# Optimization experiments

Measured on AMD Instinct MI355X. Metric: run time of the kernel, lower is better.

## Reference

```python
import jax, jax.numpy as jnp
import numpy as np

D_MODEL = 1024
NUM_HEADS = 16
D_K = D_MODEL // NUM_HEADS
SCALE = float(np.sqrt(D_K))


def setup_inputs() -> dict:
    key = jax.random.key(0)
    ks = jax.random.split(key, 12)
    B, S = 4, 2048
    s = 1.0 / np.sqrt(D_MODEL)
    inp = {
        'query': jax.random.normal(ks[0], (B, S, D_MODEL), jnp.float32),
        'key':   jax.random.normal(ks[1], (B, S, D_MODEL), jnp.float32),
        'value': jax.random.normal(ks[2], (B, S, D_MODEL), jnp.float32),
        'Wq': jax.random.normal(ks[3], (D_MODEL, D_MODEL), jnp.float32) * s,
        'bq': jax.random.normal(ks[4], (D_MODEL,), jnp.float32) * s,
        'Wk': jax.random.normal(ks[5], (D_MODEL, D_MODEL), jnp.float32) * s,
        'bk': jax.random.normal(ks[6], (D_MODEL,), jnp.float32) * s,
        'Wv': jax.random.normal(ks[7], (D_MODEL, D_MODEL), jnp.float32) * s,
        'bv': jax.random.normal(ks[8], (D_MODEL,), jnp.float32) * s,
        'Wo': jax.random.normal(ks[9], (D_MODEL, D_MODEL), jnp.float32) * s,
        'bo': jax.random.normal(ks[10], (D_MODEL,), jnp.float32) * s,
    }
    return inp


def reference(query, key, value, Wq, bq, Wk, bk, Wv, bv, Wo, bo):
    B, Sq, _ = query.shape
    Skv = key.shape[1]
    # torch Linear: x @ W.T + b
    def proj(x, W, b, S):
        y = jnp.einsum('bsd,ed->bse', x, W) + b
        return y.reshape(B, S, NUM_HEADS, D_K).transpose(0, 2, 1, 3)  # [B,H,S,dk]
    Q = proj(query, Wq, bq, Sq)
    K = proj(key, Wk, bk, Skv)
    V = proj(value, Wv, bv, Skv)
    scores = jnp.einsum('bhqd,bhkd->bhqk', Q, K) / SCALE  # [B,H,Sq,Skv]
    attn = jax.nn.softmax(scores, axis=-1)  # dropout=0 -> identity
    out = jnp.einsum('bhqk,bhkd->bhqd', attn, V)
    out = out.transpose(0, 2, 1, 3).reshape(B, Sq, D_MODEL)
    out = jnp.einsum('bsd,ed->bse', out, Wo) + bo
    return out
```

## Files before the change

kernel.cpp:

```cpp
#include <hip/hip_runtime.h>


typedef __attribute__((ext_vector_type(8))) __bf16 bf16x8;
typedef __attribute__((ext_vector_type(4))) __bf16 bf16x4;
typedef __attribute__((ext_vector_type(4))) float f32x4;

#define SCALE_FOLD 0.18033688011112043f

__device__ __forceinline__ void async_copy16(const void* g, void* lds) {
  __builtin_amdgcn_global_load_lds(
      (const __attribute__((address_space(1))) void*)g,
      (__attribute__((address_space(3))) void*)lds, 16, 0, 0);
}

template <int ROWS, int WIDTH>
__device__ __forceinline__ void stage_tile(const __bf16* __restrict__ g, int ld,
                                           __bf16* lds, int tid) {
  constexpr int CH = WIDTH / 8;
  const int wave_base = tid & ~63;
#pragma unroll
  for (int r = 0; r < ROWS * CH / 256; ++r) {
    int slot = r * 256 + tid;
    int row = slot / CH;
    int c = slot % CH;
    int gc = c ^ (row & (CH - 1));
    async_copy16(g + row * ld + gc * 8, lds + (r * 256 + wave_base) * 8);
  }
}

template <int WIDTH>
__device__ __forceinline__ bf16x8 frag_ld(const __bf16* lds, int row, int chunk) {
  return *(const bf16x8*)(lds + row * WIDTH +
                          ((chunk ^ (row & (WIDTH / 8 - 1))) << 3));
}

__global__ void cvt_all(const float* __restrict__ s0, const float* __restrict__ s1,
                        const float* __restrict__ s2, const float* __restrict__ s3,
                        const float* __restrict__ s4, const float* __restrict__ s5,
                        const float* __restrict__ s6, __bf16* d0, __bf16* d1,
                        __bf16* d2, __bf16* d3, __bf16* d4, __bf16* d5,
                        __bf16* d6, int n4_big, int n4_small) {
  const int z = blockIdx.y;
  const float* src;
  __bf16* dst;
  int n4;
  switch (z) {
    case 0: src = s0; dst = d0; n4 = n4_big; break;
    case 1: src = s1; dst = d1; n4 = n4_big; break;
    case 2: src = s2; dst = d2; n4 = n4_big; break;
    case 3: src = s3; dst = d3; n4 = n4_small; break;
    case 4: src = s4; dst = d4; n4 = n4_small; break;
    case 5: src = s5; dst = d5; n4 = n4_small; break;
    default: src = s6; dst = d6; n4 = n4_small; break;
  }
  int i = blockIdx.x * blockDim.x + threadIdx.x;
  if (i < n4) {
    float4 v = ((const float4*)src)[i];
    bf16x4 o = {(__bf16)v.x, (__bf16)v.y, (__bf16)v.z, (__bf16)v.w};
    ((bf16x4*)dst)[i] = o;
  }
}

__device__ __forceinline__ void gemm_body(const __bf16* __restrict__ A,
                                          const __bf16* __restrict__ B,
                                          const float* __restrict__ bias,
                                          void* __restrict__ out, int K,
                                          int mode, int m0, int n0,
                                          __bf16* Alds, __bf16* Blds) {
  const int tid = threadIdx.x;
  const int lane = tid & 63;
  const int w = tid >> 6;
  const int wm = w >> 1, wn = w & 1;
  const int l15 = lane & 15, quad = lane >> 4;

  f32x4 acc[4][4] = {};

  for (int k0 = 0; k0 < K; k0 += 64) {
    stage_tile<128, 64>(A + m0 * K + k0, K, Alds, tid);
    stage_tile<128, 64>(B + n0 * K + k0, K, Blds, tid);
    __syncthreads();
#pragma unroll
    for (int kc = 0; kc < 2; ++kc) {
      bf16x8 af[4], bfr[4];
#pragma unroll
      for (int mi = 0; mi < 4; ++mi)
        af[mi] = frag_ld<64>(Alds, wm * 64 + mi * 16 + l15, kc * 4 + quad);
#pragma unroll
      for (int ni = 0; ni < 4; ++ni)
        bfr[ni] = frag_ld<64>(Blds, wn * 64 + ni * 16 + l15, kc * 4 + quad);
#pragma unroll
      for (int mi = 0; mi < 4; ++mi)
#pragma unroll
        for (int ni = 0; ni < 4; ++ni)
          acc[mi][ni] = __builtin_amdgcn_mfma_f32_16x16x32_bf16(
              af[mi], bfr[ni], acc[mi][ni], 0, 0, 0);
    }
    __syncthreads();
  }

#pragma unroll
  for (int mi = 0; mi < 4; ++mi) {
#pragma unroll
    for (int i = 0; i < 4; ++i) {
      int grow = m0 + wm * 64 + mi * 16 + quad * 4 + i;
#pragma unroll
      for (int ni = 0; ni < 4; ++ni) {
        int gcol = n0 + wn * 64 + ni * 16 + l15;
        float v = acc[mi][ni][i];
        if (mode == 3) {
          v += bias[gcol];
          ((float*)out)[grow * 1024 + gcol] = v;
        } else if (mode == 2) {
          v += bias[grow];
          int h = grow >> 6, dd = grow & 63;
          int b = gcol >> 11, s = gcol & 2047;
          ((__bf16*)out)[(((b * 16 + h) * 64 + dd) * 2048) + s] = (__bf16)v;
        } else {
          v += bias[gcol];
          if (mode == 0) v *= SCALE_FOLD;
          int h = gcol >> 6, dd = gcol & 63;
          int b = grow >> 11, s = grow & 2047;
          ((__bf16*)out)[(((b * 16 + h) * 2048 + s) * 64) + dd] = (__bf16)v;
        }
      }
    }
  }
}

__global__ __launch_bounds__(256) void gemm_qkv(
    const __bf16* __restrict__ xq, const __bf16* __restrict__ xk,
    const __bf16* __restrict__ xv, const __bf16* __restrict__ wq,
    const __bf16* __restrict__ wk, const __bf16* __restrict__ wv,
    const float* __restrict__ bq, const float* __restrict__ bk,
    const float* __restrict__ bv, __bf16* Qb, __bf16* Kb, __bf16* Vtb) {
  __shared__ alignas(16) __bf16 Alds[128 * 64];
  __shared__ alignas(16) __bf16 Blds[128 * 64];
  const int z = blockIdx.z;
  if (z == 0) {
    gemm_body(xq, wq, bq, Qb, 1024, 0, blockIdx.y * 128, blockIdx.x * 128,
              Alds, Blds);
  } else if (z == 1) {
    gemm_body(xk, wk, bk, Kb, 1024, 1, blockIdx.y * 128, blockIdx.x * 128,
              Alds, Blds);
  } else {
    gemm_body(wv, xv, bv, Vtb, 1024, 2, blockIdx.x * 128, blockIdx.y * 128,
              Alds, Blds);
  }
}

__global__ __launch_bounds__(256) void gemm_out(const __bf16* __restrict__ A,
                                                const __bf16* __restrict__ B,
                                                const float* __restrict__ bias,
                                                float* __restrict__ out) {
  __shared__ alignas(16) __bf16 Alds[128 * 64];
  __shared__ alignas(16) __bf16 Blds[128 * 64];
  gemm_body(A, B, bias, out, 1024, 3, blockIdx.y * 128, blockIdx.x * 128, Alds,
            Blds);
}

__global__ __launch_bounds__(256) void attn_kernel(
    const __bf16* __restrict__ Qg, const __bf16* __restrict__ Kg,
    const __bf16* __restrict__ Vt, __bf16* __restrict__ AO) {
  __shared__ alignas(16) __bf16 Klds[2][64 * 64];
  __shared__ alignas(16) __bf16 Vlds[2][64 * 64];
  __shared__ alignas(16) __bf16 Plds[4][32 * 32];

  const int tid = threadIdx.x;
  const int lane = tid & 63;
  const int w = tid >> 6;
  const int l15 = lane & 15, quad = lane >> 4;
  const int bh = blockIdx.y;
  const int q0 = blockIdx.x * 128;
  const int S = 2048;

  const __bf16* Qbase = Qg + (size_t)bh * S * 64;
  const __bf16* Kbase = Kg + (size_t)bh * S * 64;
  const __bf16* Vbase = Vt + (size_t)bh * 64 * S;

  stage_tile<128, 64>(Qbase + q0 * 64, 64, (__bf16*)Klds, tid);
  __syncthreads();
  bf16x8 qf[2][2];
#pragma unroll
  for (int qi = 0; qi < 2; ++qi)
#pragma unroll
    for (int kc = 0; kc < 2; ++kc)
      qf[qi][kc] =
          frag_ld<64>((__bf16*)Klds, w * 32 + qi * 16 + l15, kc * 4 + quad);
  __syncthreads();

  stage_tile<64, 64>(Kbase, 64, Klds[0], tid);
  stage_tile<64, 64>(Vbase, S, Vlds[0], tid);
  __syncthreads();

  const bf16x8 ones = {__bf16(1.f), __bf16(1.f), __bf16(1.f), __bf16(1.f),
                       __bf16(1.f), __bf16(1.f), __bf16(1.f), __bf16(1.f)};

  f32x4 oacc[2][4] = {};
  f32x4 lacc[2] = {};
  __bf16* Pw = Plds[w];

  for (int mt = 0; mt < 32; ++mt) {
    const int cur = mt & 1;
    if (mt + 1 < 32) {
      stage_tile<64, 64>(Kbase + (mt + 1) * 64 * 64, 64, Klds[cur ^ 1], tid);
      stage_tile<64, 64>(Vbase + (mt + 1) * 64, S, Vlds[cur ^ 1], tid);
    }

#pragma unroll
    for (int sub = 0; sub < 2; ++sub) {
      f32x4 sacc[2][2] = {};
#pragma unroll
      for (int kc = 0; kc < 2; ++kc) {
        bf16x8 kf[2];
#pragma unroll
        for (int ci = 0; ci < 2; ++ci)
          kf[ci] =
              frag_ld<64>(Klds[cur], sub * 32 + ci * 16 + l15, kc * 4 + quad);
#pragma unroll
        for (int ci = 0; ci < 2; ++ci)
#pragma unroll
          for (int qi = 0; qi < 2; ++qi)
            sacc[ci][qi] = __builtin_amdgcn_mfma_f32_16x16x32_bf16(
                kf[ci], qf[qi][kc], sacc[ci][qi], 0, 0, 0);
      }

#pragma unroll
      for (int ci = 0; ci < 2; ++ci) {
#pragma unroll
        for (int qi = 0; qi < 2; ++qi) {
          bf16x4 pk;
#pragma unroll
          for (int i = 0; i < 4; ++i)
            pk[i] = (__bf16)__builtin_amdgcn_exp2f(sacc[ci][qi][i]);
          int qrow = qi * 16 + l15;
          int addr = qrow * 32 +
                     ((((ci << 1) + (quad >> 1)) ^ (qrow & 3)) << 3) +
                     ((quad & 1) << 2);
          *(bf16x4*)(Pw + addr) = pk;
        }
      }

      bf16x8 pf[2], vf[4];
#pragma unroll
      for (int mi = 0; mi < 2; ++mi)
        pf[mi] = frag_ld<32>(Pw, mi * 16 + l15, quad);
#pragma unroll
      for (int ni = 0; ni < 4; ++ni)
        vf[ni] = frag_ld<64>(Vlds[cur], ni * 16 + l15, sub * 4 + quad);
#pragma unroll
      for (int mi = 0; mi < 2; ++mi)
        lacc[mi] = __builtin_amdgcn_mfma_f32_16x16x32_bf16(pf[mi], ones,
                                                           lacc[mi], 0, 0, 0);
#pragma unroll
      for (int mi = 0; mi < 2; ++mi)
#pragma unroll
        for (int ni = 0; ni < 4; ++ni)
          oacc[mi][ni] = __builtin_amdgcn_mfma_f32_16x16x32_bf16(
              pf[mi], vf[ni], oacc[mi][ni], 0, 0, 0);
    }
    __syncthreads();
  }

  const int b = bh >> 4;
  const int hh = bh & 15;
#pragma unroll
  for (int mi = 0; mi < 2; ++mi) {
#pragma unroll
    for (int i = 0; i < 4; ++i) {
      int s = q0 + w * 32 + mi * 16 + quad * 4 + i;
      float inv_l = 1.f / lacc[mi][i];
#pragma unroll
      for (int ni = 0; ni < 4; ++ni) {
        int d = ni * 16 + l15;
        AO[((size_t)(b * 2048 + s)) * 1024 + hh * 64 + d] =
            (__bf16)(oacc[mi][ni][i] * inv_l);
      }
    }
  }
}

extern "C" void kernel_launch(void* const* d_in, const int* in_sizes, int n_in,
                              void* d_out, int out_size, void* d_ws,
                              size_t ws_size, hipStream_t stream) {
  const float* q_in = (const float*)d_in[0];
  const float* k_in = (const float*)d_in[1];
  const float* v_in = (const float*)d_in[2];
  const float* Wq = (const float*)d_in[3];
  const float* bq = (const float*)d_in[4];
  const float* Wk = (const float*)d_in[5];
  const float* bk = (const float*)d_in[6];
  const float* Wv = (const float*)d_in[7];
  const float* bv = (const float*)d_in[8];
  const float* Wo = (const float*)d_in[9];
  const float* bo = (const float*)d_in[10];

  const size_t SZ_X = (size_t)8192 * 1024 * 2;
  const size_t SZ_W = (size_t)1024 * 1024 * 2;
  char* p = (char*)d_ws;
  __bf16* xq = (__bf16*)p; p += SZ_X;
  __bf16* xk = (__bf16*)p; p += SZ_X;
  __bf16* xv = (__bf16*)p; p += SZ_X;
  __bf16* wqb = (__bf16*)p; p += SZ_W;
  __bf16* wkb = (__bf16*)p; p += SZ_W;
  __bf16* wvb = (__bf16*)p; p += SZ_W;
  __bf16* wob = (__bf16*)p; p += SZ_W;
  __bf16* Qb = (__bf16*)p; p += SZ_X;
  __bf16* Kb = (__bf16*)p; p += SZ_X;
  __bf16* Vtb = (__bf16*)p; p += SZ_X;
  __bf16* AOb = (__bf16*)p; p += SZ_X;

  const int nx4 = 8192 * 1024 / 4, nw4 = 1024 * 1024 / 4;
  cvt_all<<<dim3(nx4 / 256, 7), 256, 0, stream>>>(
      q_in, k_in, v_in, Wq, Wk, Wv, Wo, xq, xk, xv, wqb, wkb, wvb, wob, nx4,
      nw4);

  gemm_qkv<<<dim3(8, 64, 3), 256, 0, stream>>>(xq, xk, xv, wqb, wkb, wvb, bq,
                                               bk, bv, Qb, Kb, Vtb);

  attn_kernel<<<dim3(16, 64), 256, 0, stream>>>(Qb, Kb, Vtb, AOb);

  gemm_out<<<dim3(8, 64), 256, 0, stream>>>(AOb, wob, bo, (float*)d_out);
}
```

Baseline: 360.7 us.

## Rewrite attention as single-wave blocks with register-prefetched K/V

The attention kernel moves from 256-thread blocks that stage K/V tiles through LDS with block barriers to 64-thread single-wave blocks. Each wave handles 64 query rows, loads K and V fragments directly from global memory into registers, and double-buffers them one 32-key step ahead. The block index is remapped so that consecutive blocks hit different batch-head pairs. This removes LDS staging and __syncthreads, but the four waves that shared a K/V tile now each read it from global separately, relying on cache, and register pressure goes up.

Result: slower. 381.9 us (+5.9%).

```diff
diff --git a/kernel.cpp b/kernel.cpp
--- a/kernel.cpp
+++ b/kernel.cpp
@@ -158,116 +158,115 @@
             Blds);
 }
 
-__global__ __launch_bounds__(256) void attn_kernel(
+__global__ __launch_bounds__(64, 2) void attn_kernel(
     const __bf16* __restrict__ Qg, const __bf16* __restrict__ Kg,
     const __bf16* __restrict__ Vt, __bf16* __restrict__ AO) {
-  __shared__ alignas(16) __bf16 Klds[2][64 * 64];
-  __shared__ alignas(16) __bf16 Vlds[2][64 * 64];
-  __shared__ alignas(16) __bf16 Plds[4][32 * 32];
-
-  const int tid = threadIdx.x;
-  const int lane = tid & 63;
-  const int w = tid >> 6;
+  __shared__ alignas(16) __bf16 P[64 * 64];
+
+  const int lane = threadIdx.x;
   const int l15 = lane & 15, quad = lane >> 4;
-  const int bh = blockIdx.y;
-  const int q0 = blockIdx.x * 128;
   const int S = 2048;
 
-  const __bf16* Qbase = Qg + (size_t)bh * S * 64;
-  const __bf16* Kbase = Kg + (size_t)bh * S * 64;
-  const __bf16* Vbase = Vt + (size_t)bh * 64 * S;
-
-  stage_tile<128, 64>(Qbase + q0 * 64, 64, (__bf16*)Klds, tid);
-  __syncthreads();
-  bf16x8 qf[2][2];
-#pragma unroll
-  for (int qi = 0; qi < 2; ++qi)
+  const int bid = blockIdx.x;
+  const int bh = (bid & 7) * 8 + ((bid >> 3) & 7);
+  const int q0 = (bid >> 6) * 64;
+
+  const __bf16* Qb = Qg + (size_t)bh * S * 64 + q0 * 64;
+  const __bf16* Kb = Kg + (size_t)bh * S * 64;
+  const __bf16* Vb = Vt + (size_t)bh * 64 * S;
+
+  bf16x8 qf[4][2];
+#pragma unroll
+  for (int qi = 0; qi < 4; ++qi)
 #pragma unroll
     for (int kc = 0; kc < 2; ++kc)
       qf[qi][kc] =
-          frag_ld<64>((__bf16*)Klds, w * 32 + qi * 16 + l15, kc * 4 + quad);
-  __syncthreads();
-
-  stage_tile<64, 64>(Kbase, 64, Klds[0], tid);
-  stage_tile<64, 64>(Vbase, S, Vlds[0], tid);
-  __syncthreads();
+          *(const bf16x8*)(Qb + (qi * 16 + l15) * 64 + kc * 32 + quad * 8);
 
   const bf16x8 ones = {__bf16(1.f), __bf16(1.f), __bf16(1.f), __bf16(1.f),
                        __bf16(1.f), __bf16(1.f), __bf16(1.f), __bf16(1.f)};
 
-  f32x4 oacc[2][4] = {};
-  f32x4 lacc[2] = {};
-  __bf16* Pw = Plds[w];
-
-  for (int mt = 0; mt < 32; ++mt) {
-    const int cur = mt & 1;
-    if (mt + 1 < 32) {
-      stage_tile<64, 64>(Kbase + (mt + 1) * 64 * 64, 64, Klds[cur ^ 1], tid);
-      stage_tile<64, 64>(Vbase + (mt + 1) * 64, S, Vlds[cur ^ 1], tid);
-    }
-
-#pragma unroll
-    for (int sub = 0; sub < 2; ++sub) {
-      f32x4 sacc[2][2] = {};
-#pragma unroll
-      for (int kc = 0; kc < 2; ++kc) {
-        bf16x8 kf[2];
+  f32x4 oacc[4][4] = {};
+  f32x4 lacc[4] = {};
+
+  bf16x8 kf[2][2][2];
+  bf16x8 vf[2][4];
+
+#pragma unroll
+  for (int kc = 0; kc < 2; ++kc)
+#pragma unroll
+    for (int ci = 0; ci < 2; ++ci)
+      kf[0][kc][ci] =
+          *(const bf16x8*)(Kb + (ci * 16 + l15) * 64 + kc * 32 + quad * 8);
+#pragma unroll
+  for (int ni = 0; ni < 4; ++ni)
+    vf[0][ni] = *(const bf16x8*)(Vb + (ni * 16 + l15) * S + quad * 8);
+
+#pragma unroll 2
+  for (int t = 0; t < 64; ++t) {
+    const int cur = t & 1;
+    if (t + 1 < 64) {
+      const int kv1 = (t + 1) * 32;
+#pragma unroll
+      for (int kc = 0; kc < 2; ++kc)
 #pragma unroll
         for (int ci = 0; ci < 2; ++ci)
-          kf[ci] =
-              frag_ld<64>(Klds[cur], sub * 32 + ci * 16 + l15, kc * 4 + quad);
-#pragma unroll
-        for (int ci = 0; ci < 2; ++ci)
-#pragma unroll
-          for (int qi = 0; qi < 2; ++qi)
-            sacc[ci][qi] = __builtin_amdgcn_mfma_f32_16x16x32_bf16(
-                kf[ci], qf[qi][kc], sacc[ci][qi], 0, 0, 0);
+          kf[cur ^ 1][kc][ci] = *(const bf16x8*)(
+              Kb + (kv1 + ci * 16 + l15) * 64 + kc * 32 + quad * 8);
+#pragma unroll
+      for (int ni = 0; ni < 4; ++ni)
+        vf[cur ^ 1][ni] =
+            *(const bf16x8*)(Vb + (ni * 16 + l15) * S + kv1 + quad * 8);
+    }
+
+    f32x4 sacc[2][4] = {};
+#pragma unroll
+    for (int kc = 0; kc < 2; ++kc)
+#pragma unroll
+      for (int ci = 0; ci < 2; ++ci)
+#pragma unroll
+        for (int qi = 0; qi < 4; ++qi)
+          sacc[ci][qi] = __builtin_amdgcn_mfma_f32_16x16x32_bf16(
+              kf[cur][kc][ci], qf[qi][kc], sacc[ci][qi], 0, 0, 0);
+
+#pragma unroll
+    for (int ci = 0; ci < 2; ++ci) {
+#pragma unroll
+      for (int qi = 0; qi < 4; ++qi) {
+        bf16x4 pk;
+#pragma unroll
+        for (int i = 0; i < 4; ++i)
+          pk[i] = (__bf16)__builtin_amdgcn_exp2f(sacc[ci][qi][i]);
+        int qrow = qi * 16 + l15;
+        int chunk = 2 * ci + (quad >> 1);
+        int addr =
+            qrow * 64 + ((chunk ^ (qrow & 7)) << 3) + ((quad & 1) << 2);
+        *(bf16x4*)(P + addr) = pk;
       }
-
-#pragma unroll
-      for (int ci = 0; ci < 2; ++ci) {
-#pragma unroll
-        for (int qi = 0; qi < 2; ++qi) {
-          bf16x4 pk;
-#pragma unroll
-          for (int i = 0; i < 4; ++i)
-            pk[i] = (__bf16)__builtin_amdgcn_exp2f(sacc[ci][qi][i]);
-          int qrow = qi * 16 + l15;
-          int addr = qrow * 32 +
-                     ((((ci << 1) + (quad >> 1)) ^ (qrow & 3)) << 3) +
-                     ((quad & 1) << 2);
-          *(bf16x4*)(Pw + addr) = pk;
-        }
-      }
-
-      bf16x8 pf[2], vf[4];
-#pragma unroll
-      for (int mi = 0; mi < 2; ++mi)
-        pf[mi] = frag_ld<32>(Pw, mi * 16 + l15, quad);
+    }
+
+    bf16x8 pf[4];
+#pragma unroll
+    for (int mi = 0; mi < 4; ++mi) pf[mi] = frag_ld<64>(P, mi * 16 + l15, quad);
+#pragma unroll
+    for (int mi = 0; mi < 4; ++mi)
+      lacc[mi] = __builtin_amdgcn_mfma_f32_16x16x32_bf16(pf[mi], ones,
+                                                         lacc[mi], 0, 0, 0);
+#pragma unroll
+    for (int mi = 0; mi < 4; ++mi)
 #pragma unroll
       for (int ni = 0; ni < 4; ++ni)
-        vf[ni] = frag_ld<64>(Vlds[cur], ni * 16 + l15, sub * 4 + quad);
-#pragma unroll
-      for (int mi = 0; mi < 2; ++mi)
-        lacc[mi] = __builtin_amdgcn_mfma_f32_16x16x32_bf16(pf[mi], ones,
-                                                           lacc[mi], 0, 0, 0);
-#pragma unroll
-      for (int mi = 0; mi < 2; ++mi)
-#pragma unroll
-        for (int ni = 0; ni < 4; ++ni)
-          oacc[mi][ni] = __builtin_amdgcn_mfma_f32_16x16x32_bf16(
-              pf[mi], vf[ni], oacc[mi][ni], 0, 0, 0);
-    }
-    __syncthreads();
+        oacc[mi][ni] = __builtin_amdgcn_mfma_f32_16x16x32_bf16(
+            pf[mi], vf[cur][ni], oacc[mi][ni], 0, 0, 0);
   }
 
   const int b = bh >> 4;
   const int hh = bh & 15;
 #pragma unroll
-  for (int mi = 0; mi < 2; ++mi) {
+  for (int mi = 0; mi < 4; ++mi) {
 #pragma unroll
     for (int i = 0; i < 4; ++i) {
-      int s = q0 + w * 32 + mi * 16 + quad * 4 + i;
+      int s = q0 + mi * 16 + quad * 4 + i;
       float inv_l = 1.f / lacc[mi][i];
 #pragma unroll
       for (int ni = 0; ni < 4; ++ni) {
@@ -317,7 +316,7 @@
   gemm_qkv<<<dim3(8, 64, 3), 256, 0, stream>>>(xq, xk, xv, wqb, wkb, wvb, bq,
                                                bk, bv, Qb, Kb, Vtb);
 
-  attn_kernel<<<dim3(16, 64), 256, 0, stream>>>(Qb, Kb, Vtb, AOb);
+  attn_kernel<<<2048, 64, 0, stream>>>(Qb, Kb, Vtb, AOb);
 
   gemm_out<<<dim3(8, 64), 256, 0, stream>>>(AOb, wob, bo, (float*)d_out);
 }
```

## Remap block IDs per XCD for L2 locality and widen attention P tile

Applied to the files above, without the earlier changes.

Launches all three kernels on flattened 1D grids and remaps block IDs so that consecutive blocks on the same XCD share M-row panels in the GEMMs, or share the same batch-head in attention. The aim is better L2 reuse of K/V and weight tiles on the multi-XCD chip. The attention inner loop now computes scores for the full 64-key tile at once and writes a 32x64 P tile, which removes the two-pass sub loop but raises register and LDS use. The remap assumes round-robin dispatch of blocks across the 8 XCDs.

Result: faster. 342.5 us (-5.1%).

```diff
diff --git a/kernel.cpp b/kernel.cpp
--- a/kernel.cpp
+++ b/kernel.cpp
@@ -13,25 +13,22 @@
       (__attribute__((address_space(3))) void*)lds, 16, 0, 0);
 }
 
-template <int ROWS, int WIDTH>
+template <int ROWS>
 __device__ __forceinline__ void stage_tile(const __bf16* __restrict__ g, int ld,
                                            __bf16* lds, int tid) {
-  constexpr int CH = WIDTH / 8;
   const int wave_base = tid & ~63;
 #pragma unroll
-  for (int r = 0; r < ROWS * CH / 256; ++r) {
+  for (int r = 0; r < ROWS / 32; ++r) {
     int slot = r * 256 + tid;
-    int row = slot / CH;
-    int c = slot % CH;
-    int gc = c ^ (row & (CH - 1));
+    int row = slot >> 3;
+    int c = slot & 7;
+    int gc = c ^ (row & 7);
     async_copy16(g + row * ld + gc * 8, lds + (r * 256 + wave_base) * 8);
   }
 }
 
-template <int WIDTH>
 __device__ __forceinline__ bf16x8 frag_ld(const __bf16* lds, int row, int chunk) {
-  return *(const bf16x8*)(lds + row * WIDTH +
-                          ((chunk ^ (row & (WIDTH / 8 - 1))) << 3));
+  return *(const bf16x8*)(lds + row * 64 + ((chunk ^ (row & 7)) << 3));
 }
 
 __global__ void cvt_all(const float* __restrict__ s0, const float* __restrict__ s1,
@@ -76,18 +73,18 @@
   f32x4 acc[4][4] = {};
 
   for (int k0 = 0; k0 < K; k0 += 64) {
-    stage_tile<128, 64>(A + m0 * K + k0, K, Alds, tid);
-    stage_tile<128, 64>(B + n0 * K + k0, K, Blds, tid);
+    stage_tile<128>(A + m0 * K + k0, K, Alds, tid);
+    stage_tile<128>(B + n0 * K + k0, K, Blds, tid);
     __syncthreads();
 #pragma unroll
     for (int kc = 0; kc < 2; ++kc) {
       bf16x8 af[4], bfr[4];
 #pragma unroll
       for (int mi = 0; mi < 4; ++mi)
-        af[mi] = frag_ld<64>(Alds, wm * 64 + mi * 16 + l15, kc * 4 + quad);
+        af[mi] = frag_ld(Alds, wm * 64 + mi * 16 + l15, kc * 4 + quad);
 #pragma unroll
       for (int ni = 0; ni < 4; ++ni)
-        bfr[ni] = frag_ld<64>(Blds, wn * 64 + ni * 16 + l15, kc * 4 + quad);
+        bfr[ni] = frag_ld(Blds, wn * 64 + ni * 16 + l15, kc * 4 + quad);
 #pragma unroll
       for (int mi = 0; mi < 4; ++mi)
 #pragma unroll
@@ -127,6 +124,13 @@
   }
 }
 
+__device__ __forceinline__ void remap_xcd(int lid, int& mblk, int& nblk) {
+  int xcd = lid & 7;
+  int j = lid >> 3;
+  mblk = xcd * 8 + (j >> 3);
+  nblk = j & 7;
+}
+
 __global__ __launch_bounds__(256) void gemm_qkv(
     const __bf16* __restrict__ xq, const __bf16* __restrict__ xk,
     const __bf16* __restrict__ xv, const __bf16* __restrict__ wq,
@@ -135,16 +139,15 @@
     const float* __restrict__ bv, __bf16* Qb, __bf16* Kb, __bf16* Vtb) {
   __shared__ alignas(16) __bf16 Alds[128 * 64];
   __shared__ alignas(16) __bf16 Blds[128 * 64];
-  const int z = blockIdx.z;
+  int mblk, nblk;
+  remap_xcd(blockIdx.x, mblk, nblk);
+  const int z = blockIdx.y;
   if (z == 0) {
-    gemm_body(xq, wq, bq, Qb, 1024, 0, blockIdx.y * 128, blockIdx.x * 128,
-              Alds, Blds);
+    gemm_body(xq, wq, bq, Qb, 1024, 0, mblk * 128, nblk * 128, Alds, Blds);
   } else if (z == 1) {
-    gemm_body(xk, wk, bk, Kb, 1024, 1, blockIdx.y * 128, blockIdx.x * 128,
-              Alds, Blds);
+    gemm_body(xk, wk, bk, Kb, 1024, 1, mblk * 128, nblk * 128, Alds, Blds);
   } else {
-    gemm_body(wv, xv, bv, Vtb, 1024, 2, blockIdx.x * 128, blockIdx.y * 128,
-              Alds, Blds);
+    gemm_body(wv, xv, bv, Vtb, 1024, 2, nblk * 128, mblk * 128, Alds, Blds);
   }
 }
 
@@ -154,8 +157,9 @@
                                                 float* __restrict__ out) {
   __shared__ alignas(16) __bf16 Alds[128 * 64];
   __shared__ alignas(16) __bf16 Blds[128 * 64];
-  gemm_body(A, B, bias, out, 1024, 3, blockIdx.y * 128, blockIdx.x * 128, Alds,
-            Blds);
+  int mblk, nblk;
+  remap_xcd(blockIdx.x, mblk, nblk);
+  gemm_body(A, B, bias, out, 1024, 3, mblk * 128, nblk * 128, Alds, Blds);
 }
 
 __global__ __launch_bounds__(256) void attn_kernel(
@@ -163,21 +167,24 @@
     const __bf16* __restrict__ Vt, __bf16* __restrict__ AO) {
   __shared__ alignas(16) __bf16 Klds[2][64 * 64];
   __shared__ alignas(16) __bf16 Vlds[2][64 * 64];
-  __shared__ alignas(16) __bf16 Plds[4][32 * 32];
+  __shared__ alignas(16) __bf16 Plds[4][32 * 64];
 
   const int tid = threadIdx.x;
   const int lane = tid & 63;
   const int w = tid >> 6;
   const int l15 = lane & 15, quad = lane >> 4;
-  const int bh = blockIdx.y;
-  const int q0 = blockIdx.x * 128;
   const int S = 2048;
+
+  const int bid = blockIdx.x;
+  const int r = bid >> 3;
+  const int bh = (bid & 7) * 8 + (r & 7);
+  const int q0 = (r >> 3) * 128;
 
   const __bf16* Qbase = Qg + (size_t)bh * S * 64;
   const __bf16* Kbase = Kg + (size_t)bh * S * 64;
   const __bf16* Vbase = Vt + (size_t)bh * 64 * S;
 
-  stage_tile<128, 64>(Qbase + q0 * 64, 64, (__bf16*)Klds, tid);
+  stage_tile<128>(Qbase + q0 * 64, 64, (__bf16*)Klds, tid);
   __syncthreads();
   bf16x8 qf[2][2];
 #pragma unroll
@@ -185,11 +192,11 @@
 #pragma unroll
     for (int kc = 0; kc < 2; ++kc)
       qf[qi][kc] =
-          frag_ld<64>((__bf16*)Klds, w * 32 + qi * 16 + l15, kc * 4 + quad);
+          frag_ld((__bf16*)Klds, w * 32 + qi * 16 + l15, kc * 4 + quad);
   __syncthreads();
 
-  stage_tile<64, 64>(Kbase, 64, Klds[0], tid);
-  stage_tile<64, 64>(Vbase, S, Vlds[0], tid);
+  stage_tile<64>(Kbase, 64, Klds[0], tid);
+  stage_tile<64>(Vbase, S, Vlds[0], tid);
   __syncthreads();
 
   const bf16x8 ones = {__bf16(1.f), __bf16(1.f), __bf16(1.f), __bf16(1.f),
@@ -202,51 +209,49 @@
   for (int mt = 0; mt < 32; ++mt) {
     const int cur = mt & 1;
     if (mt + 1 < 32) {
-      stage_tile<64, 64>(Kbase + (mt + 1) * 64 * 64, 64, Klds[cur ^ 1], tid);
-      stage_tile<64, 64>(Vbase + (mt + 1) * 64, S, Vlds[cur ^ 1], tid);
-    }
-
-#pragma unroll
-    for (int sub = 0; sub < 2; ++sub) {
-      f32x4 sacc[2][2] = {};
-#pragma unroll
-      for (int kc = 0; kc < 2; ++kc) {
-        bf16x8 kf[2];
-#pragma unroll
-        for (int ci = 0; ci < 2; ++ci)
-          kf[ci] =
-              frag_ld<64>(Klds[cur], sub * 32 + ci * 16 + l15, kc * 4 + quad);
-#pragma unroll
-        for (int ci = 0; ci < 2; ++ci)
-#pragma unroll
-          for (int qi = 0; qi < 2; ++qi)
-            sacc[ci][qi] = __builtin_amdgcn_mfma_f32_16x16x32_bf16(
-                kf[ci], qf[qi][kc], sacc[ci][qi], 0, 0, 0);
+      stage_tile<64>(Kbase + (mt + 1) * 64 * 64, 64, Klds[cur ^ 1], tid);
+      stage_tile<64>(Vbase + (mt + 1) * 64, S, Vlds[cur ^ 1], tid);
+    }
+
+    f32x4 sacc[4][2] = {};
+#pragma unroll
+    for (int kc = 0; kc < 2; ++kc) {
+      bf16x8 kf[4];
+#pragma unroll
+      for (int ci = 0; ci < 4; ++ci)
+        kf[ci] = frag_ld(Klds[cur], ci * 16 + l15, kc * 4 + quad);
+#pragma unroll
+      for (int ci = 0; ci < 4; ++ci)
+#pragma unroll
+        for (int qi = 0; qi < 2; ++qi)
+          sacc[ci][qi] = __builtin_amdgcn_mfma_f32_16x16x32_bf16(
+              kf[ci], qf[qi][kc], sacc[ci][qi], 0, 0, 0);
+    }
+
+#pragma unroll
+    for (int ci = 0; ci < 4; ++ci) {
+#pragma unroll
+      for (int qi = 0; qi < 2; ++qi) {
+        bf16x4 pk;
+#pragma unroll
+        for (int i = 0; i < 4; ++i)
+          pk[i] = (__bf16)__builtin_amdgcn_exp2f(sacc[ci][qi][i]);
+        int qrow = qi * 16 + l15;
+        int chunk = 2 * ci + (quad >> 1);
+        int addr = qrow * 64 + ((chunk ^ (qrow & 7)) << 3) + ((quad & 1) << 2);
+        *(bf16x4*)(Pw + addr) = pk;
       }
-
-#pragma unroll
-      for (int ci = 0; ci < 2; ++ci) {
-#pragma unroll
-        for (int qi = 0; qi < 2; ++qi) {
-          bf16x4 pk;
-#pragma unroll
-          for (int i = 0; i < 4; ++i)
-            pk[i] = (__bf16)__builtin_amdgcn_exp2f(sacc[ci][qi][i]);
-          int qrow = qi * 16 + l15;
-          int addr = qrow * 32 +
-                     ((((ci << 1) + (quad >> 1)) ^ (qrow & 3)) << 3) +
-                     ((quad & 1) << 2);
-          *(bf16x4*)(Pw + addr) = pk;
-        }
-      }
-
+    }
+
+#pragma unroll
+    for (int kc = 0; kc < 2; ++kc) {
       bf16x8 pf[2], vf[4];
 #pragma unroll
       for (int mi = 0; mi < 2; ++mi)
-        pf[mi] = frag_ld<32>(Pw, mi * 16 + l15, quad);
+        pf[mi] = frag_ld(Pw, mi * 16 + l15, kc * 4 + quad);
 #pragma unroll
       for (int ni = 0; ni < 4; ++ni)
-        vf[ni] = frag_ld<64>(Vlds[cur], ni * 16 + l15, sub * 4 + quad);
+        vf[ni] = frag_ld(Vlds[cur], ni * 16 + l15, kc * 4 + quad);
 #pragma unroll
       for (int mi = 0; mi < 2; ++mi)
         lacc[mi] = __builtin_amdgcn_mfma_f32_16x16x32_bf16(pf[mi], ones,
@@ -314,10 +319,10 @@
       q_in, k_in, v_in, Wq, Wk, Wv, Wo, xq, xk, xv, wqb, wkb, wvb, wob, nx4,
       nw4);
 
-  gemm_qkv<<<dim3(8, 64, 3), 256, 0, stream>>>(xq, xk, xv, wqb, wkb, wvb, bq,
-                                               bk, bv, Qb, Kb, Vtb);
-
-  attn_kernel<<<dim3(16, 64), 256, 0, stream>>>(Qb, Kb, Vtb, AOb);
-
-  gemm_out<<<dim3(8, 64), 256, 0, stream>>>(AOb, wob, bo, (float*)d_out);
-}
+  gemm_qkv<<<dim3(512, 3), 256, 0, stream>>>(xq, xk, xv, wqb, wkb, wvb, bq,
+                                             bk, bv, Qb, Kb, Vtb);
+
+  attn_kernel<<<1024, 256, 0, stream>>>(Qb, Kb, Vtb, AOb);
+
+  gemm_out<<<512, 256, 0, stream>>>(AOb, wob, bo, (float*)d_out);
+}
```
